# Optimization experiments

Hardware: AMD Instinct MI355X
Metric: run time of the kernel (lower is better)

## Reference

```python
import jax, jax.numpy as jnp
import numpy as np

N_NODES = 100000
N_EDGES = 1600000
D_FEAT = 32


def setup_inputs() -> dict:
    key = jax.random.key(0)
    k1, k2, k3 = jax.random.split(key, 3)
    x = jax.random.normal(k1, (N_NODES, D_FEAT), dtype=jnp.float32)
    a = jax.random.randint(k2, (2, N_EDGES), 0, N_NODES, dtype=jnp.int64)
    e = jax.random.normal(k3, (N_EDGES,), dtype=jnp.float32)
    return {"x": x, "a": a, "e": e}


def reference(x, a, e):
    # phi: per-edge message = x[src] * e  (scalar edge weight)
    # sigma: per-target-node sum of incoming messages (0 for isolated nodes)
    src = a[0]
    tgt = a[1]
    msgs = x[src] * e[:, None]                       # [n_edges, d]
    out = jax.ops.segment_sum(msgs, tgt, num_segments=x.shape[0])  # [n_nodes, d]
    return out
```

## Files before the change

kernel.cpp:

```cpp
#include <hip/hip_runtime.h>
#include <hip/hip_bf16.h>


#define D_FEAT   32
#define SHIFT    7
#define BNODES   128
#define CHUNK    8192
#define MAXNB    1024
#define CAP      4096

__global__ void zero_out_kernel(float* __restrict__ out, int n) {
    int i = blockIdx.x * blockDim.x + threadIdx.x;
    if (i < n) out[i] = 0.0f;
}

__global__ void scatter_add_kernel(const float* __restrict__ x,
                                   const int* __restrict__ src,
                                   const int* __restrict__ tgt,
                                   const float* __restrict__ e,
                                   float* __restrict__ out,
                                   int n_edges) {
    long long gid   = (long long)blockIdx.x * blockDim.x + threadIdx.x;
    long long total = (long long)n_edges * D_FEAT;
    if (gid >= total) return;
    int edge = (int)(gid >> 5);
    int f    = (int)(gid & 31);
    float m = x[(long long)src[edge] * D_FEAT + f] * e[edge];
    atomicAdd(&out[(long long)tgt[edge] * D_FEAT + f], m);
}


__global__ __launch_bounds__(1024) void p1_hist_kernel(
        const int* __restrict__ tgt, int* __restrict__ Hg,
        int n_edges, int NB, int nchunks) {
    __shared__ int cnt[MAXNB];
    for (int i = threadIdx.x; i < NB; i += 1024) cnt[i] = 0;
    __syncthreads();
    int base = blockIdx.x * CHUNK;
    int lim  = min(base + CHUNK, n_edges);
    int n    = lim - base;
    int nv   = n >> 2;
    const int4* t4p = (const int4*)(tgt + base);
    for (int v = threadIdx.x; v < nv; v += 1024) {
        int4 t4 = t4p[v];
        atomicAdd(&cnt[t4.x >> SHIFT], 1);
        atomicAdd(&cnt[t4.y >> SHIFT], 1);
        atomicAdd(&cnt[t4.z >> SHIFT], 1);
        atomicAdd(&cnt[t4.w >> SHIFT], 1);
    }
    for (int i = base + (nv << 2) + threadIdx.x; i < lim; i += 1024)
        atomicAdd(&cnt[tgt[i] >> SHIFT], 1);
    __syncthreads();
    for (int i = threadIdx.x; i < NB; i += 1024)
        Hg[i * nchunks + blockIdx.x] = cnt[i];
}

__global__ void scan_block_kernel(int* __restrict__ data, int* __restrict__ bsum,
                                  int n) {
    __shared__ int s[256];
    int i = blockIdx.x * 256 + threadIdx.x;
    int v = (i < n) ? data[i] : 0;
    s[threadIdx.x] = v;
    __syncthreads();
    #pragma unroll
    for (int d = 1; d < 256; d <<= 1) {
        int t = (threadIdx.x >= d) ? s[threadIdx.x - d] : 0;
        __syncthreads();
        s[threadIdx.x] += t;
        __syncthreads();
    }
    if (i < n) data[i] = s[threadIdx.x] - v;
    if (threadIdx.x == 255) bsum[blockIdx.x] = s[255];
}

__global__ void scan_bsum_kernel(int* __restrict__ bsum, int nblk) {
    __shared__ int s[1024];
    int tid = threadIdx.x;
    int v = (tid < nblk) ? bsum[tid] : 0;
    s[tid] = v;
    __syncthreads();
    for (int d = 1; d < 1024; d <<= 1) {
        int t = (tid >= d) ? s[tid - d] : 0;
        __syncthreads();
        s[tid] += t;
        __syncthreads();
    }
    if (tid < nblk) bsum[tid] = s[tid] - v;
}

__global__ __launch_bounds__(1024) void p1_scatter_kernel(
        const int* __restrict__ src,
        const int* __restrict__ tgt,
        const float* __restrict__ e,
        const int* __restrict__ Hg,
        const int* __restrict__ bsum,
        int2* __restrict__ rec,
        int n_edges, int NB, int nchunks) {
    __shared__ int cur[MAXNB];
    for (int i = threadIdx.x; i < NB; i += 1024) {
        int j = i * nchunks + blockIdx.x;
        cur[i] = Hg[j] + bsum[j >> 8];
    }
    __syncthreads();
    int base = blockIdx.x * CHUNK;
    int lim  = min(base + CHUNK, n_edges);
    int n    = lim - base;
    int nv   = n >> 2;
    const int4*   s4p = (const int4*)(src + base);
    const int4*   t4p = (const int4*)(tgt + base);
    const float4* e4p = (const float4*)(e + base);
    for (int v = threadIdx.x; v < nv; v += 1024) {
        int4   s4 = s4p[v];
        int4   t4 = t4p[v];
        float4 e4 = e4p[v];
        int p0 = atomicAdd(&cur[t4.x >> SHIFT], 1);
        int p1 = atomicAdd(&cur[t4.y >> SHIFT], 1);
        int p2 = atomicAdd(&cur[t4.z >> SHIFT], 1);
        int p3 = atomicAdd(&cur[t4.w >> SHIFT], 1);
        rec[p0] = make_int2(s4.x | ((t4.x & (BNODES - 1)) << 17), __float_as_int(e4.x));
        rec[p1] = make_int2(s4.y | ((t4.y & (BNODES - 1)) << 17), __float_as_int(e4.y));
        rec[p2] = make_int2(s4.z | ((t4.z & (BNODES - 1)) << 17), __float_as_int(e4.z));
        rec[p3] = make_int2(s4.w | ((t4.w & (BNODES - 1)) << 17), __float_as_int(e4.w));
    }
    for (int i = base + (nv << 2) + threadIdx.x; i < lim; i += 1024) {
        int t = tgt[i];
        int pos = atomicAdd(&cur[t >> SHIFT], 1);
        rec[pos] = make_int2(src[i] | ((t & (BNODES - 1)) << 17),
                             __float_as_int(e[i]));
    }
}

__global__ __launch_bounds__(1024) void p2_apply_kernel(
        const float* __restrict__ x, const int2* __restrict__ rec,
        const int* __restrict__ Hg, const int* __restrict__ bsum,
        float* __restrict__ out,
        int n_edges, int n_nodes, int NB, int nchunks) {
    __shared__ int2 srt[CAP];
    __shared__ unsigned short sidx[CAP];
    __shared__ int  cnt[BNODES];
    __shared__ int  off[BNODES + 1];
    __shared__ int  cur[BNODES];
    __shared__ int  stmp[BNODES];

    int tid  = threadIdx.x;
    int b    = blockIdx.x;
    int j0   = b * nchunks;
    int base = Hg[j0] + bsum[j0 >> 8];
    int end;
    if (b + 1 < NB) {
        int j1 = (b + 1) * nchunks;
        end = Hg[j1] + bsum[j1 >> 8];
    } else {
        end = n_edges;
    }
    int nrec = end - base;

    if (nrec <= CAP) {
        if (tid < BNODES) cnt[tid] = 0;
        __syncthreads();
        for (int r = tid; r < nrec; r += 1024) {
            int2 a = rec[base + r];
            srt[r] = a;
            atomicAdd(&cnt[(a.x >> 17) & (BNODES - 1)], 1);
        }
        __syncthreads();
        int v = (tid < BNODES) ? cnt[tid] : 0;
        if (tid < BNODES) stmp[tid] = v;
        __syncthreads();
        #pragma unroll
        for (int d = 1; d < BNODES; d <<= 1) {
            int t = (tid < BNODES && tid >= d) ? stmp[tid - d] : 0;
            __syncthreads();
            if (tid < BNODES) stmp[tid] += t;
            __syncthreads();
        }
        if (tid < BNODES) { off[tid] = stmp[tid] - v; cur[tid] = stmp[tid] - v; }
        if (tid == 0) off[BNODES] = nrec;
        __syncthreads();
        for (int r = tid; r < nrec; r += 1024) {
            int ln = (srt[r].x >> 17) & (BNODES - 1);
            int pos = atomicAdd(&cur[ln], 1);
            sidx[pos] = (unsigned short)r;
        }
        __syncthreads();
        int f = tid & 31;
        int g = tid >> 5;
        for (int ln = g; ln < BNODES; ln += 32) {
            int p  = off[ln];
            int pe = off[ln + 1];
            float acc = 0.0f;
            for (; p + 3 < pe; p += 4) {
                int2 r0 = srt[sidx[p]];
                int2 r1 = srt[sidx[p + 1]];
                int2 r2 = srt[sidx[p + 2]];
                int2 r3 = srt[sidx[p + 3]];
                float v0 = x[(r0.x & 0x1FFFF) * D_FEAT + f] * __int_as_float(r0.y);
                float v1 = x[(r1.x & 0x1FFFF) * D_FEAT + f] * __int_as_float(r1.y);
                float v2 = x[(r2.x & 0x1FFFF) * D_FEAT + f] * __int_as_float(r2.y);
                float v3 = x[(r3.x & 0x1FFFF) * D_FEAT + f] * __int_as_float(r3.y);
                acc += (v0 + v1) + (v2 + v3);
            }
            for (; p < pe; ++p) {
                int2 r0 = srt[sidx[p]];
                acc += x[(r0.x & 0x1FFFF) * D_FEAT + f] * __int_as_float(r0.y);
            }
            int node = (b << SHIFT) + ln;
            if (node < n_nodes)
                out[(long long)node * D_FEAT + f] = acc;
        }
    } else {
        float* accS = (float*)srt;
        for (int i = tid; i < BNODES * D_FEAT; i += 1024) accS[i] = 0.0f;
        __syncthreads();
        int f = tid & 31;
        for (int r = base + (tid >> 5); r < end; r += 32) {
            int2 a = rec[r];
            float v = x[(a.x & 0x1FFFF) * D_FEAT + f] * __int_as_float(a.y);
            atomicAdd(&accS[((a.x >> 17) & (BNODES - 1)) * D_FEAT + f], v);
        }
        __syncthreads();
        int out0 = b << SHIFT;
        for (int i = tid; i < BNODES * D_FEAT; i += 1024) {
            int node = out0 + (i >> 5);
            if (node < n_nodes) out[(long long)out0 * D_FEAT + i] = accS[i];
        }
    }
}

extern "C" void kernel_launch(void* const* d_in, const int* in_sizes, int n_in,
                              void* d_out, int out_size, void* d_ws, size_t ws_size,
                              hipStream_t stream) {
    const float* x = (const float*)d_in[0];
    const int*   a = (const int*)d_in[1];
    const float* e = (const float*)d_in[2];

    int n_edges = in_sizes[2];
    int n_nodes = out_size / D_FEAT;
    const int* src = a;
    const int* tgt = a + n_edges;
    float* out = (float*)d_out;

    int NB        = (n_nodes + BNODES - 1) >> SHIFT;
    int nchunks   = (n_edges + CHUNK - 1) / CHUNK;
    int scan_n    = NB * nchunks;
    int nblk_scan = (scan_n + 255) / 256;

    size_t rec_bytes  = (size_t)n_edges * sizeof(int2);
    size_t hg_bytes   = (size_t)scan_n * sizeof(int);
    size_t bsum_bytes = (size_t)nblk_scan * sizeof(int);
    size_t need = rec_bytes + hg_bytes + bsum_bytes;

    bool ok = (ws_size >= need) && (NB <= MAXNB) && (nblk_scan <= 1024) &&
              (n_nodes <= (1 << 17));
    if (!ok) {
        int threads = 256;
        zero_out_kernel<<<(out_size + threads - 1) / threads, threads, 0, stream>>>(out, out_size);
        long long total = (long long)n_edges * D_FEAT;
        int blocks = (int)((total + threads - 1) / threads);
        scatter_add_kernel<<<blocks, threads, 0, stream>>>(x, src, tgt, e, out, n_edges);
        return;
    }

    char* p = (char*)d_ws;
    int2* rec  = (int2*)p; p += rec_bytes;
    int*  Hg   = (int*)p;  p += hg_bytes;
    int*  bsum = (int*)p;

    p1_hist_kernel<<<nchunks, 1024, 0, stream>>>(tgt, Hg, n_edges, NB, nchunks);
    scan_block_kernel<<<nblk_scan, 256, 0, stream>>>(Hg, bsum, scan_n);
    scan_bsum_kernel<<<1, 1024, 0, stream>>>(bsum, nblk_scan);
    p1_scatter_kernel<<<nchunks, 1024, 0, stream>>>(src, tgt, e, Hg, bsum, rec, n_edges, NB, nchunks);
    p2_apply_kernel<<<NB, 1024, 0, stream>>>(x, rec, Hg, bsum, out, n_edges, n_nodes, NB, nchunks);
}
```

Baseline: 72.54 us.

## Halve apply block size, record local ranks in registers, deepen gather unroll

```diff
diff --git a/kernel.cpp b/kernel.cpp
--- a/kernel.cpp
+++ b/kernel.cpp
@@ -7,7 +7,9 @@
 #define BNODES   128
 #define CHUNK    8192
 #define MAXNB    1024
-#define CAP      4096
+#define CAP      3072
+#define ATHR     512
+#define KMAX     (CAP / ATHR)
 
 __global__ void zero_out_kernel(float* __restrict__ out, int n) {
     int i = blockIdx.x * blockDim.x + threadIdx.x;
@@ -130,7 +132,7 @@
     }
 }
 
-__global__ __launch_bounds__(1024) void p2_apply_kernel(
+__global__ __launch_bounds__(ATHR) void p2_apply_kernel(
         const float* __restrict__ x, const int2* __restrict__ rec,
         const int* __restrict__ Hg, const int* __restrict__ bsum,
         float* __restrict__ out,
@@ -139,7 +141,6 @@
     __shared__ unsigned short sidx[CAP];
     __shared__ int  cnt[BNODES];
     __shared__ int  off[BNODES + 1];
-    __shared__ int  cur[BNODES];
     __shared__ int  stmp[BNODES];
 
     int tid  = threadIdx.x;
@@ -158,10 +159,19 @@
     if (nrec <= CAP) {
         if (tid < BNODES) cnt[tid] = 0;
         __syncthreads();
-        for (int r = tid; r < nrec; r += 1024) {
-            int2 a = rec[base + r];
-            srt[r] = a;
-            atomicAdd(&cnt[(a.x >> 17) & (BNODES - 1)], 1);
+        int myln[KMAX];
+        int myrk[KMAX];
+        #pragma unroll
+        for (int k = 0; k < KMAX; ++k) {
+            int r = tid + k * ATHR;
+            myln[k] = -1;
+            if (r < nrec) {
+                int2 a = rec[base + r];
+                srt[r] = a;
+                int ln = (a.x >> 17) & (BNODES - 1);
+                myln[k] = ln;
+                myrk[k] = atomicAdd(&cnt[ln], 1);
+            }
         }
         __syncthreads();
         int v = (tid < BNODES) ? cnt[tid] : 0;
@@ -174,31 +184,39 @@
             if (tid < BNODES) stmp[tid] += t;
             __syncthreads();
         }
-        if (tid < BNODES) { off[tid] = stmp[tid] - v; cur[tid] = stmp[tid] - v; }
+        if (tid < BNODES) off[tid] = stmp[tid] - v;
         if (tid == 0) off[BNODES] = nrec;
         __syncthreads();
-        for (int r = tid; r < nrec; r += 1024) {
-            int ln = (srt[r].x >> 17) & (BNODES - 1);
-            int pos = atomicAdd(&cur[ln], 1);
-            sidx[pos] = (unsigned short)r;
+        #pragma unroll
+        for (int k = 0; k < KMAX; ++k) {
+            if (myln[k] >= 0)
+                sidx[off[myln[k]] + myrk[k]] = (unsigned short)(tid + k * ATHR);
         }
         __syncthreads();
         int f = tid & 31;
         int g = tid >> 5;
-        for (int ln = g; ln < BNODES; ln += 32) {
+        for (int ln = g; ln < BNODES; ln += 16) {
             int p  = off[ln];
             int pe = off[ln + 1];
             float acc = 0.0f;
-            for (; p + 3 < pe; p += 4) {
+            for (; p + 7 < pe; p += 8) {
                 int2 r0 = srt[sidx[p]];
                 int2 r1 = srt[sidx[p + 1]];
                 int2 r2 = srt[sidx[p + 2]];
                 int2 r3 = srt[sidx[p + 3]];
+                int2 r4 = srt[sidx[p + 4]];
+                int2 r5 = srt[sidx[p + 5]];
+                int2 r6 = srt[sidx[p + 6]];
+                int2 r7 = srt[sidx[p + 7]];
                 float v0 = x[(r0.x & 0x1FFFF) * D_FEAT + f] * __int_as_float(r0.y);
                 float v1 = x[(r1.x & 0x1FFFF) * D_FEAT + f] * __int_as_float(r1.y);
                 float v2 = x[(r2.x & 0x1FFFF) * D_FEAT + f] * __int_as_float(r2.y);
                 float v3 = x[(r3.x & 0x1FFFF) * D_FEAT + f] * __int_as_float(r3.y);
-                acc += (v0 + v1) + (v2 + v3);
+                float v4 = x[(r4.x & 0x1FFFF) * D_FEAT + f] * __int_as_float(r4.y);
+                float v5 = x[(r5.x & 0x1FFFF) * D_FEAT + f] * __int_as_float(r5.y);
+                float v6 = x[(r6.x & 0x1FFFF) * D_FEAT + f] * __int_as_float(r6.y);
+                float v7 = x[(r7.x & 0x1FFFF) * D_FEAT + f] * __int_as_float(r7.y);
+                acc += ((v0 + v1) + (v2 + v3)) + ((v4 + v5) + (v6 + v7));
             }
             for (; p < pe; ++p) {
                 int2 r0 = srt[sidx[p]];
@@ -210,17 +228,17 @@
         }
     } else {
         float* accS = (float*)srt;
-        for (int i = tid; i < BNODES * D_FEAT; i += 1024) accS[i] = 0.0f;
+        for (int i = tid; i < BNODES * D_FEAT; i += ATHR) accS[i] = 0.0f;
         __syncthreads();
         int f = tid & 31;
-        for (int r = base + (tid >> 5); r < end; r += 32) {
+        for (int r = base + (tid >> 5); r < end; r += (ATHR >> 5)) {
             int2 a = rec[r];
             float v = x[(a.x & 0x1FFFF) * D_FEAT + f] * __int_as_float(a.y);
             atomicAdd(&accS[((a.x >> 17) & (BNODES - 1)) * D_FEAT + f], v);
         }
         __syncthreads();
         int out0 = b << SHIFT;
-        for (int i = tid; i < BNODES * D_FEAT; i += 1024) {
+        for (int i = tid; i < BNODES * D_FEAT; i += ATHR) {
             int node = out0 + (i >> 5);
             if (node < n_nodes) out[(long long)out0 * D_FEAT + i] = accS[i];
         }
@@ -270,5 +288,5 @@
     scan_block_kernel<<<nblk_scan, 256, 0, stream>>>(Hg, bsum, scan_n);
     scan_bsum_kernel<<<1, 1024, 0, stream>>>(bsum, nblk_scan);
     p1_scatter_kernel<<<nchunks, 1024, 0, stream>>>(src, tgt, e, Hg, bsum, rec, n_edges, NB, nchunks);
-    p2_apply_kernel<<<NB, 1024, 0, stream>>>(x, rec, Hg, bsum, out, n_edges, n_nodes, NB, nchunks);
-}
+    p2_apply_kernel<<<NB, ATHR, 0, stream>>>(x, rec, Hg, bsum, out, n_edges, n_nodes, NB, nchunks);
+}
```

New measurement: 68.16 us. 1.06x faster.
